# Kernel optimization log

Measured on AMD Instinct MI355X. Metric: run time of the kernel, lower is better.

## Reference

```python
import jax, jax.numpy as jnp
import numpy as np

T, B, X, Y = 24, 16, 64, 64
S, M, C = 16, 8, 8
F = S + M + C   # GRU input_size = 32
H = 32          # hidden_size


def setup_inputs() -> dict:
    key = jax.random.key(0)
    ks = jax.random.split(key, 8)
    inv = 1.0 / np.sqrt(H)
    return {
        "spatial": jax.random.normal(ks[0], (T, B, X, Y, S), dtype=jnp.float32),
        "meteorology": jax.random.normal(ks[1], (T, B, X, Y, M), dtype=jnp.float32),
        "context": jax.random.normal(ks[2], (T, B, X, Y, C), dtype=jnp.float32),
        # GRU parameters (torch layout: [3H, F] and [3H, H], gate order r,z,n)
        "W_ih": jax.random.uniform(ks[3], (3 * H, F), jnp.float32, -inv, inv),
        "W_hh": jax.random.uniform(ks[4], (3 * H, H), jnp.float32, -inv, inv),
        "b_ih": jax.random.uniform(ks[5], (3 * H,), jnp.float32, -inv, inv),
        "b_hh": jax.random.uniform(ks[6], (3 * H,), jnp.float32, -inv, inv),
        # output projection (hidden -> spatial_size)
        "W": jax.random.normal(ks[7], (H, S), dtype=jnp.float32),
    }


def reference(spatial, meteorology, context, W_ih, W_hh, b_ih, b_hh, W):
    # cat features: (T, B, X, Y, F); merge all pixels + batch into one GRU batch
    x = jnp.concatenate((spatial, meteorology, context), axis=4)
    N = B * X * Y
    x = x.reshape(T, N, F)

    # precompute input projections for all timesteps: (T, N, 3H)
    gx_all = jnp.einsum('tnf,gf->tng', x, W_ih) + b_ih

    def step(h, gx):
        gh = h @ W_hh.T + b_hh                      # (N, 3H)
        r = jax.nn.sigmoid(gx[:, :H] + gh[:, :H])
        z = jax.nn.sigmoid(gx[:, H:2 * H] + gh[:, H:2 * H])
        n = jnp.tanh(gx[:, 2 * H:] + r * gh[:, 2 * H:])
        h = (1.0 - z) * n + z * h
        return h, None

    h0 = jnp.zeros((N, H), dtype=x.dtype)
    h_final, _ = jax.lax.scan(step, h0, gx_all)     # (N, H)

    out = h_final @ W                               # (N, S)
    return out.reshape(B, X, Y, S)
```

## Files before the change

### kernel.cpp

```cpp
#include <hip/hip_runtime.h>
#include <hip/hip_bf16.h>


#define TSTEPS 24
#define NPIX 65536
#define PADW 40

typedef __attribute__((ext_vector_type(8))) short bf16x8;
typedef __attribute__((ext_vector_type(4))) float f32x4;
typedef __attribute__((ext_vector_type(4))) unsigned int u32x4;

#define MFMA16(a, b, c) __builtin_amdgcn_mfma_f32_16x16x32_bf16((a), (b), (c), 0, 0, 0)

__device__ __forceinline__ unsigned short f2bf(float f) {
  unsigned u = __builtin_bit_cast(unsigned, f);
  u += 0x7fffu + ((u >> 16) & 1u);
  return (unsigned short)(u >> 16);
}

__device__ __forceinline__ unsigned pk2(float a, float b) {
  __hip_bfloat162 h = __float22bfloat162_rn(float2{a, b});
  unsigned u;
  __builtin_memcpy(&u, &h, sizeof(u));
  return u;
}

__device__ __forceinline__ bf16x8 pack8(f32x4 a, f32x4 b) {
  u32x4 r = { pk2(a[0], a[1]), pk2(a[2], a[3]), pk2(b[0], b[1]), pk2(b[2], b[3]) };
  return __builtin_bit_cast(bf16x8, r);
}

__device__ __forceinline__ float sigmoid_(float x) {
  return __builtin_amdgcn_rcpf(1.f + __expf(-x));
}
__device__ __forceinline__ float tanh_(float x) {
  return 1.f - 2.f * __builtin_amdgcn_rcpf(__expf(2.f * x) + 1.f);
}

__device__ __forceinline__ bf16x8 relayout_h(const f32x4 h0, const f32x4 h1, int lane) {
  unsigned p00 = pk2(h0[0], h0[1]), p01 = pk2(h0[2], h0[3]);
  unsigned p10 = pk2(h1[0], h1[1]), p11 = pk2(h1[2], h1[3]);
  const int lo = (lane & 15) | ((lane & 16) << 1);
  const int hi = lo + 16;
  unsigned a0 = (unsigned)__shfl((int)p00, lo, 64);
  unsigned a1 = (unsigned)__shfl((int)p01, lo, 64);
  unsigned a2 = (unsigned)__shfl((int)p00, hi, 64);
  unsigned a3 = (unsigned)__shfl((int)p01, hi, 64);
  unsigned b0 = (unsigned)__shfl((int)p10, lo, 64);
  unsigned b1 = (unsigned)__shfl((int)p11, lo, 64);
  unsigned b2 = (unsigned)__shfl((int)p10, hi, 64);
  unsigned b3 = (unsigned)__shfl((int)p11, hi, 64);
  const bool t1 = (lane & 32) != 0;
  u32x4 d = { t1 ? b0 : a0, t1 ? b1 : a1, t1 ? b2 : a2, t1 ? b3 : a3 };
  return __builtin_bit_cast(bf16x8, d);
}

__global__ __launch_bounds__(256, 4)
void gru_fused(const float* __restrict__ spatial, const float* __restrict__ met,
               const float* __restrict__ ctx,
               const float* __restrict__ W_ih, const float* __restrict__ W_hh,
               const float* __restrict__ b_ih, const float* __restrict__ b_hh,
               const float* __restrict__ Wout, float* __restrict__ out) {
  __shared__ __align__(16) unsigned short sW[192 * PADW];
  __shared__ __align__(16) float sCB[64];
  __shared__ __align__(16) float sBIN[32];
  __shared__ __align__(16) float sBHN[32];

  const int tid = threadIdx.x;
  for (int i = tid; i < 96 * 32; i += 256) {
    int r = i >> 5, c = i & 31;
    sW[r * PADW + c] = f2bf(W_ih[i]);
    sW[(96 + r) * PADW + c] = f2bf(W_hh[i]);
  }
  if (tid < 64) sCB[tid] = b_ih[tid] + b_hh[tid];
  else if (tid < 96) sBIN[tid - 64] = b_ih[tid];
  else if (tid < 128) sBHN[tid - 96] = b_hh[tid - 32];
  __syncthreads();

  const int lane = tid & 63;
  const int col = lane & 15;
  const int q = lane >> 4;
  const int wave = blockIdx.x * 4 + (tid >> 6);
  const long p = (long)wave * 16 + col;

  f32x4 cS[4];
#pragma unroll
  for (int i = 0; i < 4; ++i) cS[i] = *(const f32x4*)&sCB[i * 16 + q * 4];
  const f32x4 cG4 = *(const f32x4*)&sBIN[q * 4];
  const f32x4 cG5 = *(const f32x4*)&sBIN[16 + q * 4];
  const f32x4 cH4 = *(const f32x4*)&sBHN[q * 4];
  const f32x4 cH5 = *(const f32x4*)&sBHN[16 + q * 4];

  const float* xptr;
  long xstride;
  if (q < 2)       { xptr = spatial + p * 16 + q * 8; xstride = (long)NPIX * 16; }
  else if (q == 2) { xptr = met + p * 8;              xstride = (long)NPIX * 8;  }
  else             { xptr = ctx + p * 8;              xstride = (long)NPIX * 8;  }

  bf16x8 bx = pack8(*(const f32x4*)xptr, *(const f32x4*)(xptr + 4));
  xptr += xstride;

  f32x4 h0 = {0.f, 0.f, 0.f, 0.f};
  f32x4 h1 = {0.f, 0.f, 0.f, 0.f};

  const int wb = col * PADW + q * 8;

#pragma unroll 2
  for (int t = 0; t < TSTEPS; ++t) {
    f32x4 xna, xnb;
    if (t < TSTEPS - 1) {
      xna = *(const f32x4*)xptr;
      xnb = *(const f32x4*)(xptr + 4);
      xptr += xstride;
    }

    bf16x8 bh = relayout_h(h0, h1, lane);

    bf16x8 a0 = *(const bf16x8*)&sW[wb];
    bf16x8 a1 = *(const bf16x8*)&sW[wb + 16 * PADW];
    bf16x8 a2 = *(const bf16x8*)&sW[wb + 32 * PADW];
    bf16x8 a3 = *(const bf16x8*)&sW[wb + 48 * PADW];
    bf16x8 a4 = *(const bf16x8*)&sW[wb + 64 * PADW];
    bf16x8 a5 = *(const bf16x8*)&sW[wb + 80 * PADW];
    bf16x8 w0 = *(const bf16x8*)&sW[wb + 96 * PADW];
    bf16x8 w1 = *(const bf16x8*)&sW[wb + 112 * PADW];
    bf16x8 w2 = *(const bf16x8*)&sW[wb + 128 * PADW];
    bf16x8 w3 = *(const bf16x8*)&sW[wb + 144 * PADW];
    bf16x8 w4 = *(const bf16x8*)&sW[wb + 160 * PADW];
    bf16x8 w5 = *(const bf16x8*)&sW[wb + 176 * PADW];

    f32x4 g0 = MFMA16(a0, bx, cS[0]);
    f32x4 g1 = MFMA16(a1, bx, cS[1]);
    f32x4 g2 = MFMA16(a2, bx, cS[2]);
    f32x4 g3 = MFMA16(a3, bx, cS[3]);
    f32x4 G4 = MFMA16(a4, bx, cG4);
    f32x4 G5 = MFMA16(a5, bx, cG5);
    f32x4 S0 = MFMA16(w0, bh, g0);
    f32x4 S1 = MFMA16(w1, bh, g1);
    f32x4 S2 = MFMA16(w2, bh, g2);
    f32x4 S3 = MFMA16(w3, bh, g3);
    f32x4 H4 = MFMA16(w4, bh, cH4);
    f32x4 H5 = MFMA16(w5, bh, cH5);

#pragma unroll
    for (int r = 0; r < 4; ++r) {
      float rv0 = sigmoid_(S0[r]);
      float rv1 = sigmoid_(S1[r]);
      float zv0 = sigmoid_(S2[r]);
      float zv1 = sigmoid_(S3[r]);
      float nv0 = tanh_(G4[r] + rv0 * H4[r]);
      float nv1 = tanh_(G5[r] + rv1 * H5[r]);
      h0[r] = nv0 + zv0 * (h0[r] - nv0);
      h1[r] = nv1 + zv1 * (h1[r] - nv1);
    }

    if (t < TSTEPS - 1) bx = pack8(xna, xnb);
  }

  bf16x8 bhf = relayout_h(h0, h1, lane);
  float w[8];
#pragma unroll
  for (int j = 0; j < 8; ++j) w[j] = Wout[(q * 8 + j) * 16 + col];
  u32x4 awp = { pk2(w[0], w[1]), pk2(w[2], w[3]), pk2(w[4], w[5]), pk2(w[6], w[7]) };
  bf16x8 aw = __builtin_bit_cast(bf16x8, awp);
  const f32x4 zero = {0.f, 0.f, 0.f, 0.f};
  f32x4 o = MFMA16(aw, bhf, zero);
  *(f32x4*)&out[p * 16 + q * 4] = o;
}

extern "C" void kernel_launch(void* const* d_in, const int* in_sizes, int n_in,
                              void* d_out, int out_size, void* d_ws, size_t ws_size,
                              hipStream_t stream) {
  const float* spatial = (const float*)d_in[0];
  const float* met     = (const float*)d_in[1];
  const float* ctx     = (const float*)d_in[2];
  const float* W_ih    = (const float*)d_in[3];
  const float* W_hh    = (const float*)d_in[4];
  const float* b_ih    = (const float*)d_in[5];
  const float* b_hh    = (const float*)d_in[6];
  const float* Wout    = (const float*)d_in[7];
  float* out = (float*)d_out;

  gru_fused<<<dim3(NPIX / 16 / 4), dim3(256), 0, stream>>>(
      spatial, met, ctx, W_ih, W_hh, b_ih, b_hh, Wout, out);
}
```

Measured before the change: 279.4 us.

## Process two independent pixel tiles per wave to interleave GRU recurrences

Each wave now handles 32 pixels as two independent 16-pixel tiles, so the two recurrence chains can interleave their MFMA and transcendental work and hide each other's latency. The LDS weight fragments are shared across both tiles. The grid is halved, launch bounds are lowered to 2 blocks per SM, and the unroll is reduced to 1 to keep register pressure under control. Hidden-state MFMAs no longer accumulate onto the input projections, so there are extra vector adds, and the kernel now has fewer waves in flight for latency hiding.

```diff
diff --git a/kernel.cpp b/kernel.cpp
--- a/kernel.cpp
+++ b/kernel.cpp
@@ -55,7 +55,7 @@
   return __builtin_bit_cast(bf16x8, d);
 }
 
-__global__ __launch_bounds__(256, 4)
+__global__ __launch_bounds__(256, 2)
 void gru_fused(const float* __restrict__ spatial, const float* __restrict__ met,
                const float* __restrict__ ctx,
                const float* __restrict__ W_ih, const float* __restrict__ W_hh,
@@ -81,7 +81,8 @@
   const int col = lane & 15;
   const int q = lane >> 4;
   const int wave = blockIdx.x * 4 + (tid >> 6);
-  const long p = (long)wave * 16 + col;
+  const long p0 = (long)wave * 32 + col;
+  const long p1 = p0 + 16;
 
   f32x4 cS[4];
 #pragma unroll
@@ -91,30 +92,38 @@
   const f32x4 cH4 = *(const f32x4*)&sBHN[q * 4];
   const f32x4 cH5 = *(const f32x4*)&sBHN[16 + q * 4];
 
-  const float* xptr;
+  const float *xp0, *xp1;
   long xstride;
-  if (q < 2)       { xptr = spatial + p * 16 + q * 8; xstride = (long)NPIX * 16; }
-  else if (q == 2) { xptr = met + p * 8;              xstride = (long)NPIX * 8;  }
-  else             { xptr = ctx + p * 8;              xstride = (long)NPIX * 8;  }
-
-  bf16x8 bx = pack8(*(const f32x4*)xptr, *(const f32x4*)(xptr + 4));
-  xptr += xstride;
-
-  f32x4 h0 = {0.f, 0.f, 0.f, 0.f};
-  f32x4 h1 = {0.f, 0.f, 0.f, 0.f};
+  if (q < 2) {
+    xp0 = spatial + p0 * 16 + q * 8; xp1 = spatial + p1 * 16 + q * 8;
+    xstride = (long)NPIX * 16;
+  } else if (q == 2) {
+    xp0 = met + p0 * 8; xp1 = met + p1 * 8; xstride = (long)NPIX * 8;
+  } else {
+    xp0 = ctx + p0 * 8; xp1 = ctx + p1 * 8; xstride = (long)NPIX * 8;
+  }
+
+  bf16x8 bx0 = pack8(*(const f32x4*)xp0, *(const f32x4*)(xp0 + 4));
+  bf16x8 bx1 = pack8(*(const f32x4*)xp1, *(const f32x4*)(xp1 + 4));
+  xp0 += xstride; xp1 += xstride;
+
+  f32x4 h0a = {0.f, 0.f, 0.f, 0.f}, h0b = {0.f, 0.f, 0.f, 0.f};
+  f32x4 h1a = {0.f, 0.f, 0.f, 0.f}, h1b = {0.f, 0.f, 0.f, 0.f};
+  const f32x4 zero = {0.f, 0.f, 0.f, 0.f};
 
   const int wb = col * PADW + q * 8;
 
-#pragma unroll 2
+#pragma unroll 1
   for (int t = 0; t < TSTEPS; ++t) {
-    f32x4 xna, xnb;
+    f32x4 xn0a, xn0b, xn1a, xn1b;
     if (t < TSTEPS - 1) {
-      xna = *(const f32x4*)xptr;
-      xnb = *(const f32x4*)(xptr + 4);
-      xptr += xstride;
+      xn0a = *(const f32x4*)xp0; xn0b = *(const f32x4*)(xp0 + 4);
+      xn1a = *(const f32x4*)xp1; xn1b = *(const f32x4*)(xp1 + 4);
+      xp0 += xstride; xp1 += xstride;
     }
 
-    bf16x8 bh = relayout_h(h0, h1, lane);
+    bf16x8 bh0 = relayout_h(h0a, h0b, lane);
+    bf16x8 bh1 = relayout_h(h1a, h1b, lane);
 
     bf16x8 a0 = *(const bf16x8*)&sW[wb];
     bf16x8 a1 = *(const bf16x8*)&sW[wb + 16 * PADW];
@@ -129,43 +138,58 @@
     bf16x8 w4 = *(const bf16x8*)&sW[wb + 160 * PADW];
     bf16x8 w5 = *(const bf16x8*)&sW[wb + 176 * PADW];
 
-    f32x4 g0 = MFMA16(a0, bx, cS[0]);
-    f32x4 g1 = MFMA16(a1, bx, cS[1]);
-    f32x4 g2 = MFMA16(a2, bx, cS[2]);
-    f32x4 g3 = MFMA16(a3, bx, cS[3]);
-    f32x4 G4 = MFMA16(a4, bx, cG4);
-    f32x4 G5 = MFMA16(a5, bx, cG5);
-    f32x4 S0 = MFMA16(w0, bh, g0);
-    f32x4 S1 = MFMA16(w1, bh, g1);
-    f32x4 S2 = MFMA16(w2, bh, g2);
-    f32x4 S3 = MFMA16(w3, bh, g3);
-    f32x4 H4 = MFMA16(w4, bh, cH4);
-    f32x4 H5 = MFMA16(w5, bh, cH5);
+    f32x4 G0[6], H0[6], G1[6], H1[6];
+    G0[0] = MFMA16(a0, bx0, cS[0]);  G1[0] = MFMA16(a0, bx1, cS[0]);
+    G0[1] = MFMA16(a1, bx0, cS[1]);  G1[1] = MFMA16(a1, bx1, cS[1]);
+    G0[2] = MFMA16(a2, bx0, cS[2]);  G1[2] = MFMA16(a2, bx1, cS[2]);
+    G0[3] = MFMA16(a3, bx0, cS[3]);  G1[3] = MFMA16(a3, bx1, cS[3]);
+    G0[4] = MFMA16(a4, bx0, cG4);    G1[4] = MFMA16(a4, bx1, cG4);
+    G0[5] = MFMA16(a5, bx0, cG5);    G1[5] = MFMA16(a5, bx1, cG5);
+    H0[0] = MFMA16(w0, bh0, zero);   H1[0] = MFMA16(w0, bh1, zero);
+    H0[1] = MFMA16(w1, bh0, zero);   H1[1] = MFMA16(w1, bh1, zero);
+    H0[2] = MFMA16(w2, bh0, zero);   H1[2] = MFMA16(w2, bh1, zero);
+    H0[3] = MFMA16(w3, bh0, zero);   H1[3] = MFMA16(w3, bh1, zero);
+    H0[4] = MFMA16(w4, bh0, cH4);    H1[4] = MFMA16(w4, bh1, cH4);
+    H0[5] = MFMA16(w5, bh0, cH5);    H1[5] = MFMA16(w5, bh1, cH5);
 
 #pragma unroll
     for (int r = 0; r < 4; ++r) {
-      float rv0 = sigmoid_(S0[r]);
-      float rv1 = sigmoid_(S1[r]);
-      float zv0 = sigmoid_(S2[r]);
-      float zv1 = sigmoid_(S3[r]);
-      float nv0 = tanh_(G4[r] + rv0 * H4[r]);
-      float nv1 = tanh_(G5[r] + rv1 * H5[r]);
-      h0[r] = nv0 + zv0 * (h0[r] - nv0);
-      h1[r] = nv1 + zv1 * (h1[r] - nv1);
+      float r00 = sigmoid_(G0[0][r] + H0[0][r]);
+      float r01 = sigmoid_(G0[1][r] + H0[1][r]);
+      float z00 = sigmoid_(G0[2][r] + H0[2][r]);
+      float z01 = sigmoid_(G0[3][r] + H0[3][r]);
+      float n00 = tanh_(G0[4][r] + r00 * H0[4][r]);
+      float n01 = tanh_(G0[5][r] + r01 * H0[5][r]);
+      h0a[r] = n00 + z00 * (h0a[r] - n00);
+      h0b[r] = n01 + z01 * (h0b[r] - n01);
+
+      float r10 = sigmoid_(G1[0][r] + H1[0][r]);
+      float r11 = sigmoid_(G1[1][r] + H1[1][r]);
+      float z10 = sigmoid_(G1[2][r] + H1[2][r]);
+      float z11 = sigmoid_(G1[3][r] + H1[3][r]);
+      float n10 = tanh_(G1[4][r] + r10 * H1[4][r]);
+      float n11 = tanh_(G1[5][r] + r11 * H1[5][r]);
+      h1a[r] = n10 + z10 * (h1a[r] - n10);
+      h1b[r] = n11 + z11 * (h1b[r] - n11);
     }
 
-    if (t < TSTEPS - 1) bx = pack8(xna, xnb);
+    if (t < TSTEPS - 1) {
+      bx0 = pack8(xn0a, xn0b);
+      bx1 = pack8(xn1a, xn1b);
+    }
   }
 
-  bf16x8 bhf = relayout_h(h0, h1, lane);
+  bf16x8 bhf0 = relayout_h(h0a, h0b, lane);
+  bf16x8 bhf1 = relayout_h(h1a, h1b, lane);
   float w[8];
 #pragma unroll
   for (int j = 0; j < 8; ++j) w[j] = Wout[(q * 8 + j) * 16 + col];
   u32x4 awp = { pk2(w[0], w[1]), pk2(w[2], w[3]), pk2(w[4], w[5]), pk2(w[6], w[7]) };
   bf16x8 aw = __builtin_bit_cast(bf16x8, awp);
-  const f32x4 zero = {0.f, 0.f, 0.f, 0.f};
-  f32x4 o = MFMA16(aw, bhf, zero);
-  *(f32x4*)&out[p * 16 + q * 4] = o;
+  f32x4 o0 = MFMA16(aw, bhf0, zero);
+  f32x4 o1 = MFMA16(aw, bhf1, zero);
+  *(f32x4*)&out[p0 * 16 + q * 4] = o0;
+  *(f32x4*)&out[p1 * 16 + q * 4] = o1;
 }
 
 extern "C" void kernel_launch(void* const* d_in, const int* in_sizes, int n_in,
@@ -181,6 +205,6 @@
   const float* Wout    = (const float*)d_in[7];
   float* out = (float*)d_out;
 
-  gru_fused<<<dim3(NPIX / 16 / 4), dim3(256), 0, stream>>>(
+  gru_fused<<<dim3(NPIX / 32 / 4), dim3(256), 0, stream>>>(
       spatial, met, ctx, W_ih, W_hh, b_ih, b_hh, Wout, out);
 }
```

Measured after the change: 233.1 us. 16.6% less time.
